# Kernel tuning notes

Measured on AMD Instinct MI355X. Metric: run time of the kernel, lower is better.

Reference implementation:

```python
import jax, jax.numpy as jnp
import numpy as np
from jax import lax

B, D, H, W = 2, 96, 96, 96
K = 3          # static upper bound on connected components (setup builds exactly 3 blobs)
CC_ITERS = 48  # >= max component diameter under 26-connectivity label propagation
V = D * H * W
BIGI = jnp.int32(V)  # sentinel label for background


def _make_target():
    # 3 well-separated spherical lesions per volume -> exactly K connected components
    centers = [(20, 20, 20), (70, 30, 60), (40, 75, 75)]
    r2 = 9 ** 2
    zz, yy, xx = np.meshgrid(np.arange(D), np.arange(H), np.arange(W), indexing='ij')
    vol = np.zeros((D, H, W), np.float32)
    for cz, cy, cx in centers:
        vol[(zz - cz) ** 2 + (yy - cy) ** 2 + (xx - cx) ** 2 <= r2] = 1.0
    return jnp.asarray(np.stack([vol, np.roll(vol, 5, axis=2)])[:, None])  # [B,1,D,H,W]


def setup_inputs() -> dict:
    key = jax.random.key(0)
    pred = jax.random.normal(key, (B, 1, D, H, W), jnp.float32)
    return {"pred": pred, "target": _make_target()}


def _connected_components(mask):
    # 26-connectivity labeling (matches skimage/cucim default for 3D).
    # Label = min flat raster index in each component, so ascending-sorted labels
    # reproduce cucim's scan-order labels 1..N (needed for tie-breaking parity).
    lab = jnp.where(mask, jnp.arange(V, dtype=jnp.int32).reshape(mask.shape), BIGI)
    for _ in range(CC_ITERS):  # fixed unroll; components have diameter << CC_ITERS
        nb = lax.reduce_window(lab, BIGI, lax.min, (3, 3, 3), (1, 1, 1), 'SAME')
        lab = jnp.where(mask, nb, BIGI)
    return lab


def _edt1d(f):
    # exact 1D squared-distance lower envelope: d[i] = min_j f[j] + (i-j)^2
    n = f.shape[-1]
    i = jnp.arange(n, dtype=jnp.float32)
    sq = (i[:, None] - i[None, :]) ** 2  # [n_out, n_in]
    return jnp.min(f[..., None, :] + sq, axis=-1)


def _squared_edt(seed):
    # exact squared Euclidean distance-to-seed via 3 separable passes
    f = jnp.where(seed, jnp.float32(0), jnp.float32(1e12))
    for ax in range(3):
        f = jnp.moveaxis(_edt1d(jnp.moveaxis(f, ax, -1)), -1, ax)
    return f


def _forward(pred, target):
    p = jax.nn.sigmoid(pred)[:, 0]  # dim==5 -> sigmoid; squeeze channel -> [B,D,H,W]
    g = target[:, 0]

    def labels(gt):
        lab = _connected_components(gt > 0.5)
        ul = jnp.unique(lab, size=K + 1, fill_value=BIGI)[:K]  # ascending = scan order
        return lab, ul

    lab, ul = jax.vmap(labels)(g)                 # lab [B,D,H,W], ul [B,K]
    valid = (ul < BIGI).astype(p.dtype)           # [B,K]
    seeds = lab[:, None] == ul[:, :, None, None, None]  # [B,K,D,H,W] bool
    # serial map over (B*K) regions keeps the [D,H,W,n] EDT intermediate to one at a time
    dists = lax.map(_squared_edt, seeds.reshape(B * K, D, H, W)).reshape(B, K, D, H, W)
    # squared vs sqrt distance: same ordering AND same ties as torch's strict '<' update;
    rmap = jnp.argmin(dists, axis=1)              # Voronoi region map [B,D,H,W]

    oh = jax.nn.one_hot(rmap, K, dtype=p.dtype)   # [B,D,H,W,K]
    inter = jnp.einsum('bdhw,bdhwk->bk', p * g, oh)
    psum = jnp.einsum('bdhw,bdhwk->bk', p, oh)
    gsum = jnp.einsum('bdhw,bdhwk->bk', g, oh)
    dice = 2.0 * inter / (psum + gsum + 1e-8)
    cnt = jnp.sum(valid, axis=1)
    mean_dice = jnp.sum(dice * valid, axis=1) / jnp.maximum(cnt, 1.0)
    loss = jnp.where(cnt > 0, 1.0 - mean_dice, 1.0)  # num_features==0 -> loss 1.0
    return jnp.mean(loss)


def reference(pred, target):
    return _forward(pred, target)
```

## Files before the change

kernel.cpp:

```cpp
#include <hip/hip_runtime.h>
#include <math.h>

#define SLICE 9216
#define VOL 884736
#define NB 2
#define KK 3
#define BIGI VOL
#define BIGP 0x3FFFFFFC
#define BIGPF 1.0e9f
#define CC_SWEEPS 3
#define NYC 4
#define NZC 4
#define NPART (NB*96*NZC)
#define MAXROW 64
#define MAXNZ 64
#define YSTR (MAXNZ*96)

#define OFF_ACT   (NB*VOL*4)
#define OFF_DISTC (2*NB*VOL*4)
#define DISTC_BYTES (NB*96*MAXNZ*96*4)
#define OFF_SMALL (OFF_DISTC + DISTC_BYTES)
#define OFF_ZMASK (OFF_SMALL + 64)
#define OFF_ROOTS (OFF_SMALL + 128)
#define OFF_MASK  (OFF_SMALL + 1024)
#define MASK_ULL  (NB*KK*96*96*2)
#define OFF_PART  (OFF_MASK + MASK_ULL*8)

__global__ void k_init(const float4* __restrict__ tgt4, int* __restrict__ lab,
                       int* __restrict__ act, int* __restrict__ small,
                       unsigned long long* __restrict__ masks) {
  int q = blockIdx.x * 256 + threadIdx.x;
  if (q < MASK_ULL) masks[q] = 0;
  if (q >= NB * VOL / 4) return;
  float4 tv = tgt4[q];
  int base = q * 4;
  int bo = (base >= VOL) ? VOL : 0;
  int4 lv;
  lv.x = (tv.x > 0.5f) ? base - bo     : BIGI;
  lv.y = (tv.y > 0.5f) ? base - bo + 1 : BIGI;
  lv.z = (tv.z > 0.5f) ? base - bo + 2 : BIGI;
  lv.w = (tv.w > 0.5f) ? base - bo + 3 : BIGI;
  ((int4*)lab)[q] = lv;
  int cnt = (lv.x != BIGI) + (lv.y != BIGI) + (lv.z != BIGI) + (lv.w != BIGI);
  if (cnt) {
    int pos = atomicAdd(&small[0], cnt);
    if (lv.x != BIGI) act[pos++] = base;
    if (lv.y != BIGI) act[pos++] = base + 1;
    if (lv.z != BIGI) act[pos++] = base + 2;
    if (lv.w != BIGI) act[pos]   = base + 3;
  }
}

__global__ void k_prop(int* __restrict__ lab, const int* __restrict__ act,
                       int* __restrict__ small, int record,
                       int* __restrict__ roots) {
  int n = small[0];
  for (int i = blockIdx.x * blockDim.x + threadIdx.x; i < n;
       i += gridDim.x * blockDim.x) {
    int idx = act[i];
    int bo = (idx >= VOL) ? VOL : 0;
    int v = idx - bo;
    int z = v / SLICE;
    int rem = v - z * SLICE;
    int y = rem / 96;
    int x = rem - y * 96;
    int* L = lab + bo;
    int z0 = z > 0 ? z - 1 : 0, z1 = z < 95 ? z + 1 : 95;
    int y0 = y > 0 ? y - 1 : 0, y1 = y < 95 ? y + 1 : 95;
    int x0 = x > 0 ? x - 1 : 0, x1 = x < 95 ? x + 1 : 95;
    int m = BIGI;
    for (int zz = z0; zz <= z1; zz++)
      for (int yy = y0; yy <= y1; yy++) {
        const int* row = L + zz * SLICE + yy * 96;
        for (int xx = x0; xx <= x1; xx++) m = min(m, row[xx]);
      }
    int m2 = L[m];
    int m3 = L[m2];
    int m4 = L[m3];
    lab[idx] = m4;
    if (record && m4 == v) {
      int b = bo ? 1 : 0;
      int pos = atomicAdd(&small[1 + b], 1);
      if (pos < 64) roots[b * 64 + pos] = v;
    }
  }
}

__global__ void k_seeds(const int* __restrict__ lab, const int* __restrict__ act,
                        const int* __restrict__ small, const int* __restrict__ roots,
                        unsigned long long* __restrict__ masks,
                        unsigned long long* __restrict__ zmg) {
  __shared__ int s_roots[128];
  __shared__ int s_ul[NB][KK];
  __shared__ unsigned long long zm[NB * 2];
  int t = threadIdx.x;
  if (t < 128) {
    int b = t >> 6, j = t & 63;
    int nr = small[1 + b]; if (nr > 64) nr = 64;
    s_roots[t] = (j < nr) ? roots[t] : 0x7fffffff;
  }
  if (t < NB * KK) s_ul[t / KK][t % KK] = -2;
  if (t < NB * 2) zm[t] = 0;
  __syncthreads();
  if (t < 128) {
    int r = s_roots[t];
    if (r != 0x7fffffff) {
      int b = t >> 6;
      int rank = 0;
      #pragma unroll
      for (int j = 0; j < 64; j++)
        rank += (s_roots[(b << 6) + j] < r) ? 1 : 0;
      if (rank < KK) s_ul[b][rank] = r;
    }
  }
  __syncthreads();
  int n = small[0];
  for (int i = blockIdx.x * 256 + t; i < n; i += gridDim.x * 256) {
    int idx = act[i];
    int b = (idx >= VOL) ? 1 : 0;
    int v = idx - (b ? VOL : 0);
    int lv = lab[idx];
    int k = (lv == s_ul[b][0]) ? 0 : (lv == s_ul[b][1]) ? 1
          : (lv == s_ul[b][2]) ? 2 : -1;
    if (k >= 0) {
      int z = v / SLICE;
      int rem = v - z * SLICE;
      int y = rem / 96;
      int x = rem - y * 96;
      unsigned long long* M =
          masks + (((size_t)(b * KK + k) * 96 + z) * 96 + y) * 2;
      if (x < 64) atomicOr(&M[0], 1ull << x);
      else        atomicOr(&M[1], 1ull << (x - 64));
      if (z < 64) atomicOr(&zm[b * 2],     1ull << z);
      else        atomicOr(&zm[b * 2 + 1], 1ull << (z - 64));
    }
  }
  __syncthreads();
  if (t < NB * 2 && zm[t]) atomicOr(&zmg[t], zm[t]);
}

__device__ __forceinline__ int row_dist(unsigned long long lo,
                                        unsigned long long hi, int x) {
  int dr, dlft;
  {
    unsigned long long rl, rh;
    if (x == 0)      { rl = lo; rh = hi; }
    else if (x < 64) { rl = (lo >> x) | (hi << (64 - x)); rh = hi >> x; }
    else             { rl = hi >> (x - 64); rh = 0; }
    dr = rl ? (__ffsll(rl) - 1) : (rh ? (63 + __ffsll(rh)) : 1000);
  }
  {
    unsigned long long ll, lh;
    if (x >= 64) { ll = lo; lh = hi & ((2ull << (x - 64)) - 1); }
    else         { ll = lo & ((2ull << x) - 1); lh = 0; }
    dlft = lh ? (x - 127 + __clzll(lh))
              : (ll ? (x - 63 + __clzll(ll)) : 1000);
  }
  return min(dr, dlft);
}

__global__ __launch_bounds__(256) void k_edt_xy(const unsigned long long* __restrict__ masks,
                                                const unsigned long long* __restrict__ zmg,
                                                float* __restrict__ distC) {
  int blk = blockIdx.x;
  int b = blk / (MAXNZ * NYC);
  int rem = blk - b * MAXNZ * NYC;
  int jj = rem / NYC;
  int yc = rem - jj * NYC;
  unsigned long long zlo = zmg[b * 2], zhi = zmg[b * 2 + 1];
  int nlo = __popcll(zlo);
  int nz = nlo + __popcll(zhi);
  if (jj >= nz) return;
  int z;
  if (jj < nlo) {
    unsigned long long w = zlo;
    for (int i = 0; i < jj; i++) w &= w - 1;
    z = __ffsll(w) - 1;
  } else {
    unsigned long long w = zhi;
    int r2 = jj - nlo;
    for (int i = 0; i < r2; i++) w &= w - 1;
    z = 64 + __ffsll(w) - 1;
  }
  __shared__ unsigned long long sM[KK * 192];
  __shared__ float pl[MAXROW * 96];
  __shared__ unsigned char vrow[96];
  __shared__ int s_n;
  int t = threadIdx.x;
  if (t == 0) s_n = 0;
  for (int i = t; i < KK * 192; i += 256) {
    int k = i / 192, r = i - k * 192;
    sM[i] = masks[((size_t)(b * KK + k) * 96 + z) * 192 + r];
  }
  __syncthreads();
  if (t < 96) {
    unsigned long long any = sM[t * 2] | sM[t * 2 + 1] | sM[192 + t * 2] |
                             sM[193 + t * 2] | sM[384 + t * 2] | sM[385 + t * 2];
    if (any) {
      int pos = atomicAdd(&s_n, 1);
      if (pos < MAXROW) vrow[pos] = (unsigned char)t;
    }
  }
  __syncthreads();
  int n = s_n; if (n > MAXROW) n = MAXROW;
  for (int i = t; i < n * 96; i += 256) {
    int j2 = i / 96, x = i - j2 * 96;
    int y = vrow[j2];
    int best = BIGP;
    #pragma unroll
    for (int k = 0; k < KK; k++) {
      unsigned long long lo = sM[k * 192 + y * 2];
      unsigned long long hi = sM[k * 192 + y * 2 + 1];
      if (lo | hi) {
        int d = row_dist(lo, hi, x);
        best = min(best, ((d * d) << 2) | k);
      }
    }
    pl[j2 * 96 + x] = (best == BIGP) ? BIGPF : (float)best;
  }
  __syncthreads();
  for (int tt = t; tt < 288; tt += 256) {
    int x = tt % 96;
    int yg = tt / 96;
    int yy0 = yc * 24 + yg * 8;
    float acc[8];
    #pragma unroll
    for (int i2 = 0; i2 < 8; i2++) acc[i2] = BIGPF;
    for (int j2 = 0; j2 < n; j2++) {
      int j = vrow[j2];
      float f = pl[j2 * 96 + x];
      float d0 = (float)(yy0 - j);
      #pragma unroll
      for (int i2 = 0; i2 < 8; i2++) {
        float dy = d0 + (float)i2;
        acc[i2] = fminf(acc[i2], __builtin_fmaf(4.f * dy, dy, f));
      }
    }
    float* DA = distC + (size_t)b * 96 * YSTR + jj * 96 + x;
    #pragma unroll
    for (int i2 = 0; i2 < 8; i2++)
      DA[(yy0 + i2) * YSTR] = acc[i2];
  }
}

__global__ __launch_bounds__(256) void k_z_fuse(const float* __restrict__ distC,
                                                const unsigned long long* __restrict__ zmg,
                                                const float* __restrict__ pred,
                                                const float* __restrict__ tgt,
                                                float* __restrict__ part,
                                                int* __restrict__ small,
                                                float* __restrict__ out) {
  int blk = blockIdx.x;
  int b = blk / (96 * NZC);
  int rem = blk - b * 96 * NZC;
  int y = rem / NZC;
  int zc = rem - y * NZC;
  __shared__ float g[MAXNZ * 96];
  __shared__ unsigned char zl[96];
  __shared__ int s_last;
  __shared__ float wsum[4][9];
  int t = threadIdx.x;
  if (t == 0) s_last = 0;
  unsigned long long zlo = zmg[b * 2], zhi = zmg[b * 2 + 1];
  int nz = __popcll(zlo) + __popcll(zhi);
  if (nz > MAXNZ) nz = MAXNZ;
  if (t < 96) {
    int set = (t < 64) ? (int)((zlo >> t) & 1) : (int)((zhi >> (t - 64)) & 1);
    if (set) {
      int jj;
      if (t < 64) jj = __popcll(zlo & ((t ? (1ull << t) : 1ull) - 1ull));
      else        jj = __popcll(zlo) + __popcll(zhi & ((1ull << (t - 64)) - 1ull));
      if (jj < MAXNZ) zl[jj] = (unsigned char)t;
    }
  }
  {
    const float4* src4 = (const float4*)(distC + (size_t)(b * 96 + y) * YSTR);
    float4* g4 = (float4*)g;
    int n4 = nz * 24;
    for (int i = t; i < n4; i += 256) g4[i] = src4[i];
  }
  __syncthreads();
  const float* P = pred + (size_t)b * VOL + y * 96;
  const float* G = tgt + (size_t)b * VOL + y * 96;
  float a0 = 0.f, a1 = 0.f, a2 = 0.f, a3 = 0.f, a4 = 0.f,
        a5 = 0.f, a6 = 0.f, a7 = 0.f, a8 = 0.f;
  for (int tt = t; tt < 288; tt += 256) {
    int x = tt % 96;
    int zg = tt / 96;
    int zz0 = zc * 24 + zg * 8;
    float pv[8], gv[8];
    #pragma unroll
    for (int i2 = 0; i2 < 8; i2++) {
      int off = (zz0 + i2) * SLICE + x;
      pv[i2] = P[off];
      gv[i2] = G[off];
    }
    float acc[8];
    #pragma unroll
    for (int i2 = 0; i2 < 8; i2++) acc[i2] = BIGPF;
    for (int jj = 0; jj < nz; jj++) {
      float f = g[jj * 96 + x];
      float d0 = (float)(zz0 - (int)zl[jj]);
      #pragma unroll
      for (int i2 = 0; i2 < 8; i2++) {
        float dz = d0 + (float)i2;
        acc[i2] = fminf(acc[i2], __builtin_fmaf(4.f * dz, dz, f));
      }
    }
    #pragma unroll
    for (int i2 = 0; i2 < 8; i2++) {
      float p = __builtin_amdgcn_rcpf(1.f + __expf(-pv[i2]));
      float gg = gv[i2];
      int kk = ((int)acc[i2]) & 3;
      float pg = p * gg;
      a0 += (kk == 0) ? pg : 0.f;
      a1 += (kk == 1) ? pg : 0.f;
      a2 += (kk == 2) ? pg : 0.f;
      a3 += (kk == 0) ? p : 0.f;
      a4 += (kk == 1) ? p : 0.f;
      a5 += (kk == 2) ? p : 0.f;
      a6 += (kk == 0) ? gg : 0.f;
      a7 += (kk == 1) ? gg : 0.f;
      a8 += (kk == 2) ? gg : 0.f;
    }
  }
  float s[9] = {a0, a1, a2, a3, a4, a5, a6, a7, a8};
  #pragma unroll
  for (int off = 32; off > 0; off >>= 1)
    #pragma unroll
    for (int q = 0; q < 9; q++) s[q] += __shfl_down(s[q], off);
  int wave = t >> 6, lane = t & 63;
  if (lane == 0) {
    #pragma unroll
    for (int q = 0; q < 9; q++) wsum[wave][q] = s[q];
  }
  __syncthreads();
  if (t < 9)
    part[blk * 9 + t] = wsum[0][t] + wsum[1][t] + wsum[2][t] + wsum[3][t];
  __syncthreads();
  if (t == 0) {
    __threadfence();
    int c = atomicAdd(&small[3], 1);
    s_last = (c == NPART - 1) ? 1 : 0;
  }
  __syncthreads();
  if (!s_last) return;
  __threadfence();
  float a[18];
  #pragma unroll
  for (int q = 0; q < 18; q++) a[q] = 0.f;
  for (int r = t; r < NPART; r += 256) {
    int bb = r / (96 * NZC);
    #pragma unroll
    for (int q = 0; q < 9; q++) a[bb * 9 + q] += part[r * 9 + q];
  }
  #pragma unroll
  for (int off = 32; off > 0; off >>= 1)
    #pragma unroll
    for (int q = 0; q < 18; q++) a[q] += __shfl_down(a[q], off);
  __shared__ float fs[4][18];
  if (lane == 0) {
    #pragma unroll
    for (int q = 0; q < 18; q++) fs[wave][q] = a[q];
  }
  __syncthreads();
  if (t == 0) {
    float tot[18];
    #pragma unroll
    for (int q = 0; q < 18; q++)
      tot[q] = fs[0][q] + fs[1][q] + fs[2][q] + fs[3][q];
    float loss = 0.f;
    for (int bb = 0; bb < NB; bb++) {
      int cnt = small[1 + bb];
      if (cnt > KK) cnt = KK;
      float ds = 0.f;
      for (int k = 0; k < cnt; k++) {
        float inter = tot[bb * 9 + k];
        float ps = tot[bb * 9 + 3 + k];
        float gs = tot[bb * 9 + 6 + k];
        ds += 2.f * inter / (ps + gs + 1e-8f);
      }
      float mean = ds / fmaxf((float)cnt, 1.f);
      loss += (cnt > 0) ? (1.f - mean) : 1.f;
    }
    out[0] = loss * 0.5f;
  }
}

extern "C" void kernel_launch(void* const* d_in, const int* in_sizes, int n_in,
                              void* d_out, int out_size, void* d_ws, size_t ws_size,
                              hipStream_t stream) {
  const float* pred = (const float*)d_in[0];
  const float* tgt  = (const float*)d_in[1];
  float* out = (float*)d_out;

  char* ws = (char*)d_ws;
  int* lab   = (int*)(ws);
  int* act   = (int*)(ws + OFF_ACT);
  float* distC = (float*)(ws + OFF_DISTC);
  int* small = (int*)(ws + OFF_SMALL);
  unsigned long long* zmg = (unsigned long long*)(ws + OFF_ZMASK);
  int* roots = (int*)(ws + OFF_ROOTS);
  unsigned long long* masks = (unsigned long long*)(ws + OFF_MASK);
  float* part = (float*)(ws + OFF_PART);

  hipMemsetAsync(ws + OFF_SMALL, 0, 128, stream);
  k_init<<<(NB * VOL / 4 + 255) / 256, 256, 0, stream>>>(
      (const float4*)tgt, lab, act, small, masks);
  for (int it = 0; it < CC_SWEEPS; it++)
    k_prop<<<96, 256, 0, stream>>>(lab, act, small, it == CC_SWEEPS - 1 ? 1 : 0, roots);
  k_seeds<<<96, 256, 0, stream>>>(lab, act, small, roots, masks, zmg);
  k_edt_xy<<<NB * MAXNZ * NYC, 256, 0, stream>>>(masks, zmg, distC);
  k_z_fuse<<<NB * 96 * NZC, 256, 0, stream>>>(distC, zmg, pred, tgt, part, small, out);
}
```

Before: 141.9 us.

## Fuse seed-mask building into EDT kernel and drop k_seeds pass

Removes the separate k_seeds kernel and its global bitmask buffer. Each k_edt_xy block now ranks the component roots itself, scans its z-slice of labels and builds the per-component row bitmasks in shared memory. The z-occupancy mask moves into k_init, which works from foreground voxels rather than labeled components. This saves a launch, the global mask zeroing and the global atomics, but every block (including the NYC duplicates) rereads a full label slice, and the z-mask may now include slices whose voxels are not in the top-K components.

```diff
diff --git a/kernel.cpp b/kernel.cpp
--- a/kernel.cpp
+++ b/kernel.cpp
@@ -22,33 +22,41 @@
 #define OFF_SMALL (OFF_DISTC + DISTC_BYTES)
 #define OFF_ZMASK (OFF_SMALL + 64)
 #define OFF_ROOTS (OFF_SMALL + 128)
-#define OFF_MASK  (OFF_SMALL + 1024)
-#define MASK_ULL  (NB*KK*96*96*2)
-#define OFF_PART  (OFF_MASK + MASK_ULL*8)
+#define OFF_PART  (OFF_SMALL + 4096)
+
 
 __global__ void k_init(const float4* __restrict__ tgt4, int* __restrict__ lab,
                        int* __restrict__ act, int* __restrict__ small,
-                       unsigned long long* __restrict__ masks) {
-  int q = blockIdx.x * 256 + threadIdx.x;
-  if (q < MASK_ULL) masks[q] = 0;
-  if (q >= NB * VOL / 4) return;
-  float4 tv = tgt4[q];
-  int base = q * 4;
-  int bo = (base >= VOL) ? VOL : 0;
-  int4 lv;
-  lv.x = (tv.x > 0.5f) ? base - bo     : BIGI;
-  lv.y = (tv.y > 0.5f) ? base - bo + 1 : BIGI;
-  lv.z = (tv.z > 0.5f) ? base - bo + 2 : BIGI;
-  lv.w = (tv.w > 0.5f) ? base - bo + 3 : BIGI;
-  ((int4*)lab)[q] = lv;
-  int cnt = (lv.x != BIGI) + (lv.y != BIGI) + (lv.z != BIGI) + (lv.w != BIGI);
-  if (cnt) {
-    int pos = atomicAdd(&small[0], cnt);
-    if (lv.x != BIGI) act[pos++] = base;
-    if (lv.y != BIGI) act[pos++] = base + 1;
-    if (lv.z != BIGI) act[pos++] = base + 2;
-    if (lv.w != BIGI) act[pos]   = base + 3;
-  }
+                       unsigned long long* __restrict__ zmg) {
+  __shared__ unsigned long long zm[4];
+  int t = threadIdx.x;
+  if (t < 4) zm[t] = 0;
+  __syncthreads();
+  int q = blockIdx.x * 256 + t;
+  if (q < NB * VOL / 4) {
+    float4 tv = tgt4[q];
+    int base = q * 4;
+    int bo = (base >= VOL) ? VOL : 0;
+    int4 lv;
+    lv.x = (tv.x > 0.5f) ? base - bo     : BIGI;
+    lv.y = (tv.y > 0.5f) ? base - bo + 1 : BIGI;
+    lv.z = (tv.z > 0.5f) ? base - bo + 2 : BIGI;
+    lv.w = (tv.w > 0.5f) ? base - bo + 3 : BIGI;
+    ((int4*)lab)[q] = lv;
+    int cnt = (lv.x != BIGI) + (lv.y != BIGI) + (lv.z != BIGI) + (lv.w != BIGI);
+    if (cnt) {
+      int b = bo ? 1 : 0;
+      int z = (base - bo) / SLICE;
+      atomicOr(&zm[b * 2 + (z >= 64)], 1ull << (z & 63));
+      int pos = atomicAdd(&small[0], cnt);
+      if (lv.x != BIGI) act[pos++] = base;
+      if (lv.y != BIGI) act[pos++] = base + 1;
+      if (lv.z != BIGI) act[pos++] = base + 2;
+      if (lv.w != BIGI) act[pos]   = base + 3;
+    }
+  }
+  __syncthreads();
+  if (t < 4 && zm[t]) atomicOr(&zmg[t], zm[t]);
 }
 
 __global__ void k_prop(int* __restrict__ lab, const int* __restrict__ act,
@@ -86,59 +94,6 @@
   }
 }
 
-__global__ void k_seeds(const int* __restrict__ lab, const int* __restrict__ act,
-                        const int* __restrict__ small, const int* __restrict__ roots,
-                        unsigned long long* __restrict__ masks,
-                        unsigned long long* __restrict__ zmg) {
-  __shared__ int s_roots[128];
-  __shared__ int s_ul[NB][KK];
-  __shared__ unsigned long long zm[NB * 2];
-  int t = threadIdx.x;
-  if (t < 128) {
-    int b = t >> 6, j = t & 63;
-    int nr = small[1 + b]; if (nr > 64) nr = 64;
-    s_roots[t] = (j < nr) ? roots[t] : 0x7fffffff;
-  }
-  if (t < NB * KK) s_ul[t / KK][t % KK] = -2;
-  if (t < NB * 2) zm[t] = 0;
-  __syncthreads();
-  if (t < 128) {
-    int r = s_roots[t];
-    if (r != 0x7fffffff) {
-      int b = t >> 6;
-      int rank = 0;
-      #pragma unroll
-      for (int j = 0; j < 64; j++)
-        rank += (s_roots[(b << 6) + j] < r) ? 1 : 0;
-      if (rank < KK) s_ul[b][rank] = r;
-    }
-  }
-  __syncthreads();
-  int n = small[0];
-  for (int i = blockIdx.x * 256 + t; i < n; i += gridDim.x * 256) {
-    int idx = act[i];
-    int b = (idx >= VOL) ? 1 : 0;
-    int v = idx - (b ? VOL : 0);
-    int lv = lab[idx];
-    int k = (lv == s_ul[b][0]) ? 0 : (lv == s_ul[b][1]) ? 1
-          : (lv == s_ul[b][2]) ? 2 : -1;
-    if (k >= 0) {
-      int z = v / SLICE;
-      int rem = v - z * SLICE;
-      int y = rem / 96;
-      int x = rem - y * 96;
-      unsigned long long* M =
-          masks + (((size_t)(b * KK + k) * 96 + z) * 96 + y) * 2;
-      if (x < 64) atomicOr(&M[0], 1ull << x);
-      else        atomicOr(&M[1], 1ull << (x - 64));
-      if (z < 64) atomicOr(&zm[b * 2],     1ull << z);
-      else        atomicOr(&zm[b * 2 + 1], 1ull << (z - 64));
-    }
-  }
-  __syncthreads();
-  if (t < NB * 2 && zm[t]) atomicOr(&zmg[t], zm[t]);
-}
-
 __device__ __forceinline__ int row_dist(unsigned long long lo,
                                         unsigned long long hi, int x) {
   int dr, dlft;
@@ -159,7 +114,9 @@
   return min(dr, dlft);
 }
 
-__global__ __launch_bounds__(256) void k_edt_xy(const unsigned long long* __restrict__ masks,
+__global__ __launch_bounds__(256) void k_edt_xy(const int* __restrict__ lab,
+                                                const int* __restrict__ small,
+                                                const int* __restrict__ roots,
                                                 const unsigned long long* __restrict__ zmg,
                                                 float* __restrict__ distC) {
   int blk = blockIdx.x;
@@ -186,11 +143,39 @@
   __shared__ float pl[MAXROW * 96];
   __shared__ unsigned char vrow[96];
   __shared__ int s_n;
+  __shared__ int s_roots[64];
+  __shared__ int s_ul[KK];
   int t = threadIdx.x;
+  if (t < 64) {
+    int nr = small[1 + b]; if (nr > 64) nr = 64;
+    s_roots[t] = (t < nr) ? roots[b * 64 + t] : 0x7fffffff;
+  }
+  if (t < KK) s_ul[t] = -2;
   if (t == 0) s_n = 0;
-  for (int i = t; i < KK * 192; i += 256) {
-    int k = i / 192, r = i - k * 192;
-    sM[i] = masks[((size_t)(b * KK + k) * 96 + z) * 192 + r];
+  for (int i = t; i < KK * 192; i += 256) sM[i] = 0;
+  __syncthreads();
+  if (t < 64) {
+    int r = s_roots[t];
+    if (r != 0x7fffffff) {
+      int rank = 0;
+      #pragma unroll
+      for (int j = 0; j < 64; j++)
+        rank += (s_roots[j] < r) ? 1 : 0;
+      if (rank < KK) s_ul[rank] = r;
+    }
+  }
+  __syncthreads();
+  const int* Lb = lab + b * VOL + z * SLICE;
+  int u0 = s_ul[0], u1 = s_ul[1], u2 = s_ul[2];
+  for (int i = t; i < SLICE; i += 256) {
+    int lvv = Lb[i];
+    if (lvv != BIGI) {
+      int k = (lvv == u0) ? 0 : (lvv == u1) ? 1 : (lvv == u2) ? 2 : -1;
+      if (k >= 0) {
+        int yy = i / 96, xx = i - yy * 96;
+        atomicOr(&sM[k * 192 + yy * 2 + (xx >> 6)], 1ull << (xx & 63));
+      }
+    }
   }
   __syncthreads();
   if (t < 96) {
@@ -401,15 +386,13 @@
   int* small = (int*)(ws + OFF_SMALL);
   unsigned long long* zmg = (unsigned long long*)(ws + OFF_ZMASK);
   int* roots = (int*)(ws + OFF_ROOTS);
-  unsigned long long* masks = (unsigned long long*)(ws + OFF_MASK);
   float* part = (float*)(ws + OFF_PART);
 
   hipMemsetAsync(ws + OFF_SMALL, 0, 128, stream);
   k_init<<<(NB * VOL / 4 + 255) / 256, 256, 0, stream>>>(
-      (const float4*)tgt, lab, act, small, masks);
+      (const float4*)tgt, lab, act, small, zmg);
   for (int it = 0; it < CC_SWEEPS; it++)
     k_prop<<<96, 256, 0, stream>>>(lab, act, small, it == CC_SWEEPS - 1 ? 1 : 0, roots);
-  k_seeds<<<96, 256, 0, stream>>>(lab, act, small, roots, masks, zmg);
-  k_edt_xy<<<NB * MAXNZ * NYC, 256, 0, stream>>>(masks, zmg, distC);
+  k_edt_xy<<<NB * MAXNZ * NYC, 256, 0, stream>>>(lab, small, roots, zmg, distC);
   k_z_fuse<<<NB * 96 * NZC, 256, 0, stream>>>(distC, zmg, pred, tgt, part, small, out);
 }
```

Measured after the change: 154.2 us. +8.7%, slower.
